# Performance work log

Measured on AMD Instinct MI355X. Metric: run time of the kernel, lower is better.

## Reference

```python
import jax, jax.numpy as jnp
import numpy as np

B, T, D = 2, 2048, 1024
H, DK, DV = 16, 64, 64
FF = 4096


def setup_inputs() -> dict:
    key = jax.random.key(0)
    ks = jax.random.split(key, 10)
    s = 0.02
    return {
        "x": jax.random.normal(ks[0], (B, T, D), dtype=jnp.float32),
        "Wq": jax.random.normal(ks[1], (H, D, DK), dtype=jnp.float32) * s,
        "Wk": jax.random.normal(ks[2], (H, D, DK), dtype=jnp.float32) * s,
        "Wv": jax.random.normal(ks[3], (H, D, DV), dtype=jnp.float32) * s,
        "Wo": jax.random.normal(ks[4], (D, D), dtype=jnp.float32) * s,
        "W1": jax.random.normal(ks[5], (D, FF), dtype=jnp.float32) * s,
        "b1": jnp.zeros((FF,), dtype=jnp.float32),
        "W2": jax.random.normal(ks[6], (FF, D), dtype=jnp.float32) * s,
        "b2": jnp.zeros((D,), dtype=jnp.float32),
    }


def _meanstd_norm(y):
    # torch: mean(-1), std(-1) with Bessel correction (ddof=1)
    mean = jnp.mean(y, axis=-1, keepdims=True)
    var = jnp.sum((y - mean) ** 2, axis=-1, keepdims=True) / (y.shape[-1] - 1)
    return (y - mean) / jnp.sqrt(var)


def reference(x, Wq, Wk, Wv, Wo, W1, b1, W2, b2):
    dk = Wq.shape[-1]
    # per-head projections: (B,T,D) x (H,D,dk) -> (B,H,T,dk)
    q = jnp.einsum('btd,hdk->bhtk', x, Wq)
    k = jnp.einsum('btd,hdk->bhtk', x, Wk)
    v = jnp.einsum('btd,hdv->bhtv', x, Wv)
    scores = jnp.einsum('bhqk,bhsk->bhqs', q, k) / np.sqrt(dk)
    # NOTE: softmax over dim=-2 (query axis), as in the original module
    attn = jax.nn.softmax(scores, axis=-2)
    o = jnp.einsum('bhqs,bhsv->bhqv', attn, v)  # (B,H,T,DV)
    o = o.transpose(0, 2, 1, 3).reshape(o.shape[0], o.shape[2], -1)  # (B,T,H*DV)
    o = o @ Wo
    out1 = _meanstd_norm(o + x)
    ff = jax.nn.relu(out1 @ W1 + b1) @ W2 + b2
    out2 = _meanstd_norm(ff + out1)
    return out2
```

## Files before the change

kernel.cpp:

```cpp
#include <hip/hip_runtime.h>
#include <hip/hip_bf16.h>
#include <math.h>

#define B_  2
#define T_  2048
#define D_  1024
#define H_  16
#define DK_ 64
#define FF_ 4096
#define BT_ (B_*T_)

typedef __attribute__((ext_vector_type(8))) short bf16x8;
typedef __attribute__((ext_vector_type(4))) float f32x4;

__device__ __forceinline__ ushort f2bf(float f) {
    __hip_bfloat16 h = __float2bfloat16(f);
    return *reinterpret_cast<ushort*>(&h);
}
__device__ __forceinline__ float bf2f(ushort u) {
    __hip_bfloat16 h;
    *reinterpret_cast<ushort*>(&h) = u;
    return __bfloat162float(h);
}

__device__ __forceinline__ void g2l16(const ushort* g, ushort* l) {
    __builtin_amdgcn_global_load_lds(
        (const __attribute__((address_space(1))) void*)g,
        (__attribute__((address_space(3))) void*)l, 16, 0, 0);
}

__global__ __launch_bounds__(256) void cvt_bf16_kernel(
    const float* __restrict__ in, ushort* __restrict__ out, int n)
{
    int i = (blockIdx.x * 256 + threadIdx.x) * 4;
    if (i >= n) return;
    float4 v = *(const float4*)(in + i);
    ushort4 o;
    o.x = f2bf(v.x); o.y = f2bf(v.y); o.z = f2bf(v.z); o.w = f2bf(v.w);
    *(ushort4*)(out + i) = o;
}

__global__ __launch_bounds__(256) void transpose_bf16_kernel(
    const float* __restrict__ in, ushort* __restrict__ out,
    int K, int N, long in_bstride, long out_bstride)
{
    __shared__ float t[32][33];
    const float* ib = in + (size_t)blockIdx.z * in_bstride;
    ushort* ob = out + (size_t)blockIdx.z * out_bstride;
    int n0 = blockIdx.x * 32, k0 = blockIdx.y * 32;
    int tid = threadIdx.x;
    int r = tid >> 3, c4 = (tid & 7) * 4;
    float4 v = *(const float4*)(ib + (size_t)(k0 + r) * N + n0 + c4);
    t[r][c4] = v.x; t[r][c4+1] = v.y; t[r][c4+2] = v.z; t[r][c4+3] = v.w;
    __syncthreads();
    int n = tid >> 3, kc = (tid & 7) * 4;
    ushort4 o;
    o.x = f2bf(t[kc+0][n]); o.y = f2bf(t[kc+1][n]);
    o.z = f2bf(t[kc+2][n]); o.w = f2bf(t[kc+3][n]);
    *(ushort4*)(ob + (size_t)(n0 + n) * K + k0 + kc) = o;
}

template<int OUT_BF16>
__global__ __launch_bounds__(256, 2) void gemm_ntw_kernel(
    const ushort* __restrict__ A, int lda,
    const ushort* __restrict__ Bt, int ldb,
    void* __restrict__ C, int ldc, int K,
    const float* __restrict__ bias,
    const float* __restrict__ resid, int relu)
{
    __shared__ __attribute__((aligned(16))) ushort As[2][4][128][8];
    __shared__ __attribute__((aligned(16))) ushort Bs[2][4][256][8];

    int nwg  = gridDim.x * gridDim.y;
    int orig = blockIdx.y * gridDim.x + blockIdx.x;
    int work = (orig & 7) * (nwg >> 3) + (orig >> 3);
    int bx = work % gridDim.x, by = work / gridDim.x;

    int row0 = by * 128, col0 = bx * 256;
    int tid = threadIdx.x;
    int w = tid >> 6, l = tid & 63;
    int wr = (w >> 1) * 64, wc = (w & 1) * 128;

    int m0 = tid & 127, kc0 = tid >> 7;
    const ushort* gA = A  + (size_t)(row0 + m0) * lda + kc0 * 8;
    const ushort* gB = Bt + (size_t)(col0 + tid) * ldb;

    f32x4 acc[4][8];
    #pragma unroll
    for (int i = 0; i < 4; ++i)
        #pragma unroll
        for (int j = 0; j < 8; ++j) acc[i][j] = (f32x4){0.f, 0.f, 0.f, 0.f};

    const int NT = K >> 5;
    g2l16(gA,      &As[0][kc0    ][m0][0]);
    g2l16(gA + 16, &As[0][kc0 + 2][m0][0]);
    #pragma unroll
    for (int p = 0; p < 4; ++p)
        g2l16(gB + p*8, &Bs[0][p][tid][0]);
    __syncthreads();

    int cur = 0;
    for (int t = 0; t < NT; ++t) {
        if (t + 1 < NT) {
            int k0 = (t + 1) << 5;
            g2l16(gA + k0,      &As[cur ^ 1][kc0    ][m0][0]);
            g2l16(gA + k0 + 16, &As[cur ^ 1][kc0 + 2][m0][0]);
            #pragma unroll
            for (int p = 0; p < 4; ++p)
                g2l16(gB + k0 + p*8, &Bs[cur ^ 1][p][tid][0]);
        }
        int kc = l >> 4;
        bf16x8 bfr[8];
        #pragma unroll
        for (int j = 0; j < 8; ++j)
            bfr[j] = *(const bf16x8*)&Bs[cur][kc][wc + j*16 + (l & 15)][0];
        #pragma unroll
        for (int i = 0; i < 4; ++i) {
            bf16x8 a = *(const bf16x8*)&As[cur][kc][wr + i*16 + (l & 15)][0];
            #pragma unroll
            for (int j = 0; j < 8; ++j)
                acc[i][j] = __builtin_amdgcn_mfma_f32_16x16x32_bf16(
                    a, bfr[j], acc[i][j], 0, 0, 0);
        }
        __syncthreads();
        cur ^= 1;
    }

    #pragma unroll
    for (int i = 0; i < 4; ++i) {
        int rbase = row0 + wr + i*16 + (l >> 4) * 4;
        #pragma unroll
        for (int j = 0; j < 8; ++j) {
            int col = col0 + wc + j*16 + (l & 15);
            float bv = bias ? bias[col] : 0.f;
            #pragma unroll
            for (int r = 0; r < 4; ++r) {
                int row = rbase + r;
                float val = acc[i][j][r] + bv;
                if (resid) val += resid[(size_t)row * ldc + col];
                if (relu)  val = fmaxf(val, 0.f);
                if (OUT_BF16) ((ushort*)C)[(size_t)row * ldc + col] = f2bf(val);
                else          ((float*)C)[(size_t)row * ldc + col]  = val;
            }
        }
    }
}

template<int OUT_BF16>
__global__ __launch_bounds__(256) void gemm_nt_kernel(
    const ushort* __restrict__ A, int lda,
    const ushort* __restrict__ Bt, int ldb,
    void* __restrict__ C, int ldc, int K,
    const float* __restrict__ bias,
    const float* __restrict__ resid, int relu,
    long aZoff, long bZoff, long cZoff)
{
    __shared__ __attribute__((aligned(16))) ushort As[2][4][128][8];
    __shared__ __attribute__((aligned(16))) ushort Bs[2][4][128][8];

    A  += (size_t)blockIdx.z * aZoff;
    Bt += (size_t)blockIdx.z * bZoff;
    char* Cb = (char*)C + (size_t)blockIdx.z * cZoff * (OUT_BF16 ? 2 : 4);

    int nwg  = gridDim.x * gridDim.y;
    int orig = blockIdx.y * gridDim.x + blockIdx.x;
    int work = (orig & 7) * (nwg >> 3) + (orig >> 3);
    int bx = work % gridDim.x, by = work / gridDim.x;

    int row0 = by * 128, col0 = bx * 128;
    int tid = threadIdx.x;
    int w = tid >> 6, l = tid & 63;
    int wr = (w >> 1) * 64, wc = (w & 1) * 64;

    int m0 = tid & 127, kc0 = tid >> 7;
    const ushort* ga0 = A  + (size_t)(row0 + m0) * lda + kc0 * 8;
    const ushort* gb0 = Bt + (size_t)(col0 + m0) * ldb + kc0 * 8;

    f32x4 acc[4][4];
    #pragma unroll
    for (int i = 0; i < 4; ++i)
        #pragma unroll
        for (int j = 0; j < 4; ++j) acc[i][j] = (f32x4){0.f, 0.f, 0.f, 0.f};

    const int NT = K >> 5;
    g2l16(ga0,      &As[0][kc0    ][m0][0]);
    g2l16(ga0 + 16, &As[0][kc0 + 2][m0][0]);
    g2l16(gb0,      &Bs[0][kc0    ][m0][0]);
    g2l16(gb0 + 16, &Bs[0][kc0 + 2][m0][0]);
    __syncthreads();

    int cur = 0;
    for (int t = 0; t < NT; ++t) {
        if (t + 1 < NT) {
            int k0 = (t + 1) << 5;
            g2l16(ga0 + k0,      &As[cur ^ 1][kc0    ][m0][0]);
            g2l16(ga0 + k0 + 16, &As[cur ^ 1][kc0 + 2][m0][0]);
            g2l16(gb0 + k0,      &Bs[cur ^ 1][kc0    ][m0][0]);
            g2l16(gb0 + k0 + 16, &Bs[cur ^ 1][kc0 + 2][m0][0]);
        }
        int kc = l >> 4;
        bf16x8 af[4], bfr[4];
        #pragma unroll
        for (int i = 0; i < 4; ++i)
            af[i] = *(const bf16x8*)&As[cur][kc][wr + i*16 + (l & 15)][0];
        #pragma unroll
        for (int j = 0; j < 4; ++j)
            bfr[j] = *(const bf16x8*)&Bs[cur][kc][wc + j*16 + (l & 15)][0];
        #pragma unroll
        for (int i = 0; i < 4; ++i)
            #pragma unroll
            for (int j = 0; j < 4; ++j)
                acc[i][j] = __builtin_amdgcn_mfma_f32_16x16x32_bf16(
                    af[i], bfr[j], acc[i][j], 0, 0, 0);
        __syncthreads();
        cur ^= 1;
    }

    #pragma unroll
    for (int i = 0; i < 4; ++i) {
        int rbase = row0 + wr + i*16 + (l >> 4) * 4;
        #pragma unroll
        for (int j = 0; j < 4; ++j) {
            int col = col0 + wc + j*16 + (l & 15);
            float bv = bias ? bias[col] : 0.f;
            #pragma unroll
            for (int r = 0; r < 4; ++r) {
                int row = rbase + r;
                float val = acc[i][j][r] + bv;
                if (resid) val += resid[(size_t)row * ldc + col];
                if (relu)  val = fmaxf(val, 0.f);
                if (OUT_BF16) ((ushort*)Cb)[(size_t)row * ldc + col] = f2bf(val);
                else          ((float*)Cb)[(size_t)row * ldc + col]  = val;
            }
        }
    }
}

__global__ __launch_bounds__(256) void csumv_kernel(
    const ushort* __restrict__ qkv, ushort* __restrict__ vt)
{
    int bh = blockIdx.y, b = bh >> 4, h = bh & 15;
    int s0 = blockIdx.x * 128;
    const ushort* qb = qkv + (size_t)b * T_ * 3072 + h * 64;
    const ushort* kb = qb + 1024;
    const ushort* vb = qb + 2048;
    __shared__ __attribute__((aligned(16))) ushort Ks[8][128][8];
    __shared__ __attribute__((aligned(16))) ushort Qs[8][64][8];
    __shared__ float csl[128];
    __shared__ float t[64][65];
    int tid = threadIdx.x, w = tid >> 6, l = tid & 63;
    int scol = w * 32;

    #pragma unroll
    for (int p = 0; p < 4; ++p) {
        int idx = tid + p * 256;
        int s = idx & 127, kc = idx >> 7;
        *(uint4*)&Ks[kc][s][0] =
            *(const uint4*)(kb + (size_t)(s0 + s) * 3072 + kc * 8);
    }
    float cs[2] = {0.f, 0.f};
    for (int qt = 0; qt < T_ / 64; ++qt) {
        __syncthreads();
        #pragma unroll
        for (int p = 0; p < 2; ++p) {
            int idx = tid + p * 256;
            int qq = idx & 63, kc = idx >> 6;
            *(uint4*)&Qs[kc][qq][0] =
                *(const uint4*)(qb + (size_t)(qt*64 + qq) * 3072 + kc * 8);
        }
        __syncthreads();
        bf16x8 af[4][2], bfr[2][2];
        #pragma unroll
        for (int qi = 0; qi < 4; ++qi)
            #pragma unroll
            for (int ks = 0; ks < 2; ++ks)
                af[qi][ks] = *(const bf16x8*)&Qs[ks*4 + (l>>4)][qi*16 + (l & 15)][0];
        #pragma unroll
        for (int sj = 0; sj < 2; ++sj)
            #pragma unroll
            for (int ks = 0; ks < 2; ++ks)
                bfr[sj][ks] = *(const bf16x8*)&Ks[ks*4 + (l>>4)][scol + sj*16 + (l & 15)][0];
        #pragma unroll
        for (int qi = 0; qi < 4; ++qi)
            #pragma unroll
            for (int sj = 0; sj < 2; ++sj) {
                f32x4 d = (f32x4){0.f, 0.f, 0.f, 0.f};
                #pragma unroll
                for (int ks = 0; ks < 2; ++ks)
                    d = __builtin_amdgcn_mfma_f32_16x16x32_bf16(
                        af[qi][ks], bfr[sj][ks], d, 0, 0, 0);
                cs[sj] += __expf(d[0]*0.125f) + __expf(d[1]*0.125f)
                        + __expf(d[2]*0.125f) + __expf(d[3]*0.125f);
            }
    }
    #pragma unroll
    for (int sj = 0; sj < 2; ++sj) {
        float v = cs[sj];
        v += __shfl_down(v, 32, 64);
        v += __shfl_down(v, 16, 64);
        if (l < 16) csl[scol + sj*16 + l] = v;
    }
    __syncthreads();

    #pragma unroll
    for (int p2 = 0; p2 < 2; ++p2) {
        int sb = s0 + p2 * 64;
        #pragma unroll
        for (int p = 0; p < 2; ++p) {
            int idx = tid + p * 256;
            int s = idx >> 3, c0 = (idx & 7) * 8;
            uint4 raw = *(const uint4*)(vb + (size_t)(sb + s) * 3072 + c0);
            float rc = 1.0f / csl[p2 * 64 + s];
            ushort* u = (ushort*)&raw;
            #pragma unroll
            for (int i = 0; i < 8; ++i) t[s][c0 + i] = bf2f(u[i]) * rc;
        }
        __syncthreads();
        #pragma unroll
        for (int p = 0; p < 2; ++p) {
            int idx = tid + p * 256;
            int dv = idx >> 3, sc = (idx & 7) * 8;
            ushort o[8];
            #pragma unroll
            for (int i = 0; i < 8; ++i) o[i] = f2bf(t[sc + i][dv]);
            *(uint4*)(vt + ((size_t)bh * 64 + dv) * T_ + sb + sc) = *(uint4*)o;
        }
        __syncthreads();
    }
}

__global__ __launch_bounds__(256) void attn_pv_kernel(
    const ushort* __restrict__ qkv, const ushort* __restrict__ vt,
    ushort* __restrict__ attn_o)
{
    int bh = blockIdx.y, b = bh >> 4, h = bh & 15;
    int q0 = blockIdx.x * 64;
    const ushort* qb = qkv + (size_t)b * T_ * 3072 + h * 64;
    const ushort* kb = qb + 1024;
    const ushort* vtb = vt + (size_t)bh * 64 * T_;
    __shared__ __attribute__((aligned(16))) ushort Qs[8][64][8];
    __shared__ __attribute__((aligned(16))) ushort Ks[8][64][8];
    __shared__ __attribute__((aligned(16))) ushort Vs[8][64][8];
    __shared__ __attribute__((aligned(16))) ushort Es[8][64][8];
    int tid = threadIdx.x, w = tid >> 6, l = tid & 63;
    int qw = w * 16;

    #pragma unroll
    for (int p = 0; p < 2; ++p) {
        int idx = tid + p * 256;
        int qq = idx & 63, kc = idx >> 6;
        *(uint4*)&Qs[kc][qq][0] =
            *(const uint4*)(qb + (size_t)(q0 + qq) * 3072 + kc * 8);
    }
    __syncthreads();
    bf16x8 qf[2];
    #pragma unroll
    for (int ks = 0; ks < 2; ++ks)
        qf[ks] = *(const bf16x8*)&Qs[ks*4 + (l>>4)][qw + (l & 15)][0];

    f32x4 oacc[4];
    #pragma unroll
    for (int j = 0; j < 4; ++j) oacc[j] = (f32x4){0.f, 0.f, 0.f, 0.f};

    for (int st = 0; st < T_ / 64; ++st) {
        int s0 = st * 64;
        __syncthreads();
        #pragma unroll
        for (int p = 0; p < 2; ++p) {
            int idx = tid + p * 256;
            int rr = idx & 63, kc = idx >> 6;
            *(uint4*)&Ks[kc][rr][0] =
                *(const uint4*)(kb + (size_t)(s0 + rr) * 3072 + kc * 8);
            *(uint4*)&Vs[kc][rr][0] =
                *(const uint4*)(vtb + (size_t)rr * T_ + s0 + kc * 8);
        }
        __syncthreads();
        #pragma unroll
        for (int sj = 0; sj < 4; ++sj) {
            f32x4 d = (f32x4){0.f, 0.f, 0.f, 0.f};
            #pragma unroll
            for (int ks = 0; ks < 2; ++ks) {
                bf16x8 kf = *(const bf16x8*)&Ks[ks*4 + (l>>4)][sj*16 + (l & 15)][0];
                d = __builtin_amdgcn_mfma_f32_16x16x32_bf16(qf[ks], kf, d, 0, 0, 0);
            }
            #pragma unroll
            for (int r = 0; r < 4; ++r) {
                int qq = qw + (l>>4)*4 + r;
                int ss = sj*16 + (l & 15);
                Es[ss >> 3][qq][ss & 7] = f2bf(__expf(d[r] * 0.125f));
            }
        }
        bf16x8 ef[2];
        #pragma unroll
        for (int ks = 0; ks < 2; ++ks)
            ef[ks] = *(const bf16x8*)&Es[ks*4 + (l>>4)][qw + (l & 15)][0];
        #pragma unroll
        for (int j = 0; j < 4; ++j)
            #pragma unroll
            for (int ks = 0; ks < 2; ++ks) {
                bf16x8 vf = *(const bf16x8*)&Vs[ks*4 + (l>>4)][j*16 + (l & 15)][0];
                oacc[j] = __builtin_amdgcn_mfma_f32_16x16x32_bf16(ef[ks], vf, oacc[j], 0, 0, 0);
            }
    }
    #pragma unroll
    for (int j = 0; j < 4; ++j)
        #pragma unroll
        for (int r = 0; r < 4; ++r) {
            int qq = q0 + qw + (l>>4)*4 + r;
            int dv = j*16 + (l & 15);
            attn_o[(size_t)(b*T_ + qq) * 1024 + h*64 + dv] = f2bf(oacc[j][r]);
        }
}

__device__ __forceinline__ float block_reduce_sum_256(float v, float* tmp)
{
    #pragma unroll
    for (int off = 32; off; off >>= 1) v += __shfl_down(v, off, 64);
    int lane = threadIdx.x & 63, w = threadIdx.x >> 6;
    __syncthreads();
    if (lane == 0) tmp[w] = v;
    __syncthreads();
    return tmp[0] + tmp[1] + tmp[2] + tmp[3];
}

template<int Z>
__global__ __launch_bounds__(256) void normZ_fused_kernel(
    const ushort* __restrict__ parts, long zoff,
    const float* __restrict__ bias, const float* __restrict__ resid,
    float* __restrict__ outf, ushort* __restrict__ outb)
{
    __shared__ float tmp[4];
    int row = blockIdx.x;
    int tid = threadIdx.x;
    int c0 = tid * 4;
    size_t idx = (size_t)row * D_ + c0;
    float vals[4] = {0.f, 0.f, 0.f, 0.f};
    #pragma unroll
    for (int z = 0; z < Z; ++z) {
        ushort4 p = *(const ushort4*)&parts[idx + (size_t)z * zoff];
        vals[0] += bf2f(p.x); vals[1] += bf2f(p.y);
        vals[2] += bf2f(p.z); vals[3] += bf2f(p.w);
    }
    float4 rv = *(const float4*)&resid[idx];
    vals[0] += rv.x; vals[1] += rv.y; vals[2] += rv.z; vals[3] += rv.w;
    if (bias) {
        float4 bv = *(const float4*)&bias[c0];
        vals[0] += bv.x; vals[1] += bv.y; vals[2] += bv.z; vals[3] += bv.w;
    }
    float s = vals[0] + vals[1] + vals[2] + vals[3];
    s = block_reduce_sum_256(s, tmp);
    float m = s * (1.0f / (float)D_);
    float sq = 0.f;
    #pragma unroll
    for (int i = 0; i < 4; ++i) { float c = vals[i] - m; sq += c * c; }
    sq = block_reduce_sum_256(sq, tmp);
    float rs = rsqrtf(sq * (1.0f / (float)(D_ - 1)));
    float4 o;
    o.x = (vals[0] - m) * rs; o.y = (vals[1] - m) * rs;
    o.z = (vals[2] - m) * rs; o.w = (vals[3] - m) * rs;
    *(float4*)&outf[idx] = o;
    if (outb) {
        ushort4 ob;
        ob.x = f2bf(o.x); ob.y = f2bf(o.y); ob.z = f2bf(o.z); ob.w = f2bf(o.w);
        *(ushort4*)&outb[idx] = ob;
    }
}

extern "C" void kernel_launch(void* const* d_in, const int* in_sizes, int n_in,
                              void* d_out, int out_size, void* d_ws, size_t ws_size,
                              hipStream_t stream)
{
    const float* x  = (const float*)d_in[0];
    const float* Wq = (const float*)d_in[1];
    const float* Wk = (const float*)d_in[2];
    const float* Wv = (const float*)d_in[3];
    const float* Wo = (const float*)d_in[4];
    const float* W1 = (const float*)d_in[5];
    const float* b1 = (const float*)d_in[6];
    const float* W2 = (const float*)d_in[7];
    const float* b2 = (const float*)d_in[8];
    float* out = (float*)d_out;

    const size_t MB = (size_t)1 << 20;
    char* base = (char*)d_ws;
    ushort* qkv    = (ushort*)(base +   0*MB);
    ushort* hid    = (ushort*)(base +   0*MB);
    ushort* xb     = (ushort*)(base +  24*MB);
    ushort* W2t    = (ushort*)(base +  32*MB);
    ushort* Wqkvt  = (ushort*)(base +  40*MB);
    ushort* wpart  = (ushort*)(base +  40*MB);
    ushort* vt     = (ushort*)(base +  46*MB);
    ushort* Wot    = (ushort*)(base +  55*MB);
    ushort* W1t    = (ushort*)(base +  57*MB);
    ushort* attn_o = (ushort*)(base +  65*MB);
    ushort* wopart = (ushort*)(base +  73*MB);
    ushort* out1b  = (ushort*)(base +  89*MB);
    float*  out1f  = (float*) (base +  97*MB);

    cvt_bf16_kernel<<<dim3(BT_*D_/1024), 256, 0, stream>>>(x, xb, BT_*D_);
    transpose_bf16_kernel<<<dim3(2, 32, 16), 256, 0, stream>>>(
        Wq, Wqkvt + 0*1048576, 1024, 64, 65536, 65536);
    transpose_bf16_kernel<<<dim3(2, 32, 16), 256, 0, stream>>>(
        Wk, Wqkvt + 1*1048576, 1024, 64, 65536, 65536);
    transpose_bf16_kernel<<<dim3(2, 32, 16), 256, 0, stream>>>(
        Wv, Wqkvt + 2*1048576, 1024, 64, 65536, 65536);
    transpose_bf16_kernel<<<dim3(32, 32, 1), 256, 0, stream>>>(
        Wo, Wot, 1024, 1024, 0, 0);
    transpose_bf16_kernel<<<dim3(128, 32, 1), 256, 0, stream>>>(
        W1, W1t, 1024, 4096, 0, 0);
    transpose_bf16_kernel<<<dim3(32, 128, 1), 256, 0, stream>>>(
        W2, W2t, 4096, 1024, 0, 0);

    gemm_ntw_kernel<1><<<dim3(3072/256, 4096/128), 256, 0, stream>>>(
        xb, 1024, Wqkvt, 1024, qkv, 3072, 1024, nullptr, nullptr, 0);
    csumv_kernel<<<dim3(T_/128, B_*H_), 256, 0, stream>>>(qkv, vt);
    attn_pv_kernel<<<dim3(T_/64, B_*H_), 256, 0, stream>>>(qkv, vt, attn_o);
    gemm_nt_kernel<1><<<dim3(1024/128, 4096/128, 2), 256, 0, stream>>>(
        attn_o, 1024, Wot, 1024, wopart, 1024, 512, nullptr, nullptr, 0,
        512, 512, (long)4096*1024);
    normZ_fused_kernel<2><<<dim3(BT_), 256, 0, stream>>>(
        wopart, (long)4096*1024, nullptr, x, out1f, out1b);
    gemm_ntw_kernel<1><<<dim3(4096/256, 4096/128), 256, 0, stream>>>(
        out1b, 1024, W1t, 1024, hid, 4096, 1024, b1, nullptr, 1);
    gemm_nt_kernel<1><<<dim3(1024/128, 4096/128, 2), 256, 0, stream>>>(
        hid, 4096, W2t, 4096, wpart, 1024, 2048, nullptr, nullptr, 0,
        2048, 2048, (long)4096*1024);
    normZ_fused_kernel<2><<<dim3(BT_), 256, 0, stream>>>(
        wpart, (long)4096*1024, b2, out1f, out, nullptr);
}
```

Before: 390.7 us.

## Double-buffer attention K/V/Q tiles with async loads and widen query tile

Both attention kernels now prefetch the next K/V (or Q) tile into a second LDS buffer with g2l16 asynchronous global-to-LDS copies while the current tile is computed. This replaces the two barriers per iteration with one and overlaps memory latency with MFMA and exp work. attn_pv also handles 128 queries per block, two 16-row query tiles per wave, with Q fragments read straight from global into registers. This doubles reuse of each staged K/V tile and halves the grid, at the cost of more LDS and registers per block and fewer blocks to spread across CUs.

```diff
diff --git a/kernel.cpp b/kernel.cpp
--- a/kernel.cpp
+++ b/kernel.cpp
@@ -245,11 +245,12 @@
     const ushort* kb = qb + 1024;
     const ushort* vb = qb + 2048;
     __shared__ __attribute__((aligned(16))) ushort Ks[8][128][8];
-    __shared__ __attribute__((aligned(16))) ushort Qs[8][64][8];
+    __shared__ __attribute__((aligned(16))) ushort Qs[2][8][64][8];
     __shared__ float csl[128];
     __shared__ float t[64][65];
     int tid = threadIdx.x, w = tid >> 6, l = tid & 63;
     int scol = w * 32;
+    int qq0 = l, kcA = w, kcB = w + 4;
 
     #pragma unroll
     for (int p = 0; p < 4; ++p) {
@@ -258,23 +259,24 @@
         *(uint4*)&Ks[kc][s][0] =
             *(const uint4*)(kb + (size_t)(s0 + s) * 3072 + kc * 8);
     }
+    g2l16(qb + (size_t)qq0 * 3072 + kcA * 8, &Qs[0][kcA][qq0][0]);
+    g2l16(qb + (size_t)qq0 * 3072 + kcB * 8, &Qs[0][kcB][qq0][0]);
+    __syncthreads();
+
     float cs[2] = {0.f, 0.f};
+    int cur = 0;
     for (int qt = 0; qt < T_ / 64; ++qt) {
-        __syncthreads();
-        #pragma unroll
-        for (int p = 0; p < 2; ++p) {
-            int idx = tid + p * 256;
-            int qq = idx & 63, kc = idx >> 6;
-            *(uint4*)&Qs[kc][qq][0] =
-                *(const uint4*)(qb + (size_t)(qt*64 + qq) * 3072 + kc * 8);
-        }
-        __syncthreads();
+        if (qt + 1 < T_ / 64) {
+            const ushort* qn = qb + (size_t)((qt + 1) * 64 + qq0) * 3072;
+            g2l16(qn + kcA * 8, &Qs[cur ^ 1][kcA][qq0][0]);
+            g2l16(qn + kcB * 8, &Qs[cur ^ 1][kcB][qq0][0]);
+        }
         bf16x8 af[4][2], bfr[2][2];
         #pragma unroll
         for (int qi = 0; qi < 4; ++qi)
             #pragma unroll
             for (int ks = 0; ks < 2; ++ks)
-                af[qi][ks] = *(const bf16x8*)&Qs[ks*4 + (l>>4)][qi*16 + (l & 15)][0];
+                af[qi][ks] = *(const bf16x8*)&Qs[cur][ks*4 + (l>>4)][qi*16 + (l & 15)][0];
         #pragma unroll
         for (int sj = 0; sj < 2; ++sj)
             #pragma unroll
@@ -292,6 +294,8 @@
                 cs[sj] += __expf(d[0]*0.125f) + __expf(d[1]*0.125f)
                         + __expf(d[2]*0.125f) + __expf(d[3]*0.125f);
             }
+        __syncthreads();
+        cur ^= 1;
     }
     #pragma unroll
     for (int sj = 0; sj < 2; ++sj) {
@@ -334,82 +338,95 @@
     ushort* __restrict__ attn_o)
 {
     int bh = blockIdx.y, b = bh >> 4, h = bh & 15;
-    int q0 = blockIdx.x * 64;
+    int q0 = blockIdx.x * 128;
     const ushort* qb = qkv + (size_t)b * T_ * 3072 + h * 64;
     const ushort* kb = qb + 1024;
     const ushort* vtb = vt + (size_t)bh * 64 * T_;
-    __shared__ __attribute__((aligned(16))) ushort Qs[8][64][8];
-    __shared__ __attribute__((aligned(16))) ushort Ks[8][64][8];
-    __shared__ __attribute__((aligned(16))) ushort Vs[8][64][8];
-    __shared__ __attribute__((aligned(16))) ushort Es[8][64][8];
+    __shared__ __attribute__((aligned(16))) ushort Ks[2][8][64][8];
+    __shared__ __attribute__((aligned(16))) ushort Vs[2][8][64][8];
+    __shared__ __attribute__((aligned(16))) ushort Es[8][128][8];
     int tid = threadIdx.x, w = tid >> 6, l = tid & 63;
-    int qw = w * 16;
-
-    #pragma unroll
-    for (int p = 0; p < 2; ++p) {
-        int idx = tid + p * 256;
-        int qq = idx & 63, kc = idx >> 6;
-        *(uint4*)&Qs[kc][qq][0] =
-            *(const uint4*)(qb + (size_t)(q0 + qq) * 3072 + kc * 8);
-    }
-    __syncthreads();
-    bf16x8 qf[2];
-    #pragma unroll
-    for (int ks = 0; ks < 2; ++ks)
-        qf[ks] = *(const bf16x8*)&Qs[ks*4 + (l>>4)][qw + (l & 15)][0];
-
-    f32x4 oacc[4];
-    #pragma unroll
-    for (int j = 0; j < 4; ++j) oacc[j] = (f32x4){0.f, 0.f, 0.f, 0.f};
-
-    for (int st = 0; st < T_ / 64; ++st) {
-        int s0 = st * 64;
+    int wq = w * 32;
+
+    int kcA = w, kcB = w + 4;
+
+    bf16x8 qf[2][2];
+    #pragma unroll
+    for (int qt = 0; qt < 2; ++qt)
+        #pragma unroll
+        for (int ks = 0; ks < 2; ++ks)
+            qf[qt][ks] = *(const bf16x8*)(qb
+                + (size_t)(q0 + wq + qt*16 + (l & 15)) * 3072
+                + (ks*4 + (l >> 4)) * 8);
+
+    f32x4 oacc[2][4];
+    #pragma unroll
+    for (int qt = 0; qt < 2; ++qt)
+        #pragma unroll
+        for (int j = 0; j < 4; ++j) oacc[qt][j] = (f32x4){0.f, 0.f, 0.f, 0.f};
+
+    const int NT = T_ / 64;
+    g2l16(kb + (size_t)l * 3072 + kcA * 8, &Ks[0][kcA][l][0]);
+    g2l16(kb + (size_t)l * 3072 + kcB * 8, &Ks[0][kcB][l][0]);
+    g2l16(vtb + (size_t)l * T_ + kcA * 8,  &Vs[0][kcA][l][0]);
+    g2l16(vtb + (size_t)l * T_ + kcB * 8,  &Vs[0][kcB][l][0]);
+    __syncthreads();
+
+    int cur = 0;
+    for (int st = 0; st < NT; ++st) {
+        if (st + 1 < NT) {
+            int s1 = (st + 1) * 64;
+            g2l16(kb + (size_t)(s1 + l) * 3072 + kcA * 8, &Ks[cur^1][kcA][l][0]);
+            g2l16(kb + (size_t)(s1 + l) * 3072 + kcB * 8, &Ks[cur^1][kcB][l][0]);
+            g2l16(vtb + (size_t)l * T_ + s1 + kcA * 8,    &Vs[cur^1][kcA][l][0]);
+            g2l16(vtb + (size_t)l * T_ + s1 + kcB * 8,    &Vs[cur^1][kcB][l][0]);
+        }
+        #pragma unroll
+        for (int qt = 0; qt < 2; ++qt)
+            #pragma unroll
+            for (int sj = 0; sj < 4; ++sj) {
+                f32x4 d = (f32x4){0.f, 0.f, 0.f, 0.f};
+                #pragma unroll
+                for (int ks = 0; ks < 2; ++ks) {
+                    bf16x8 kf = *(const bf16x8*)&Ks[cur][ks*4 + (l>>4)][sj*16 + (l & 15)][0];
+                    d = __builtin_amdgcn_mfma_f32_16x16x32_bf16(qf[qt][ks], kf, d, 0, 0, 0);
+                }
+                #pragma unroll
+                for (int r = 0; r < 4; ++r) {
+                    int qq = wq + qt*16 + (l>>4)*4 + r;
+                    int ss = sj*16 + (l & 15);
+                    Es[ss >> 3][qq][ss & 7] = f2bf(__expf(d[r] * 0.125f));
+                }
+            }
+        #pragma unroll
+        for (int qt = 0; qt < 2; ++qt) {
+            bf16x8 ef[2];
+            #pragma unroll
+            for (int ks = 0; ks < 2; ++ks)
+                ef[ks] = *(const bf16x8*)&Es[ks*4 + (l>>4)][wq + qt*16 + (l & 15)][0];
+            #pragma unroll
+            for (int j = 0; j < 4; ++j)
+                #pragma unroll
+                for (int ks = 0; ks < 2; ++ks) {
+                    bf16x8 vf = *(const bf16x8*)&Vs[cur][ks*4 + (l>>4)][j*16 + (l & 15)][0];
+                    oacc[qt][j] = __builtin_amdgcn_mfma_f32_16x16x32_bf16(
+                        ef[ks], vf, oacc[qt][j], 0, 0, 0);
+                }
+        }
         __syncthreads();
-        #pragma unroll
-        for (int p = 0; p < 2; ++p) {
-            int idx = tid + p * 256;
-            int rr = idx & 63, kc = idx >> 6;
-            *(uint4*)&Ks[kc][rr][0] =
-                *(const uint4*)(kb + (size_t)(s0 + rr) * 3072 + kc * 8);
-            *(uint4*)&Vs[kc][rr][0] =
-                *(const uint4*)(vtb + (size_t)rr * T_ + s0 + kc * 8);
-        }
-        __syncthreads();
-        #pragma unroll
-        for (int sj = 0; sj < 4; ++sj) {
-            f32x4 d = (f32x4){0.f, 0.f, 0.f, 0.f};
-            #pragma unroll
-            for (int ks = 0; ks < 2; ++ks) {
-                bf16x8 kf = *(const bf16x8*)&Ks[ks*4 + (l>>4)][sj*16 + (l & 15)][0];
-                d = __builtin_amdgcn_mfma_f32_16x16x32_bf16(qf[ks], kf, d, 0, 0, 0);
+        cur ^= 1;
+    }
+
+    #pragma unroll
+    for (int qt = 0; qt < 2; ++qt)
+        #pragma unroll
+        for (int j = 0; j < 4; ++j)
+            #pragma unroll
+            for (int r = 0; r < 4; ++r) {
+                int qq = q0 + wq + qt*16 + (l>>4)*4 + r;
+                int dv = j*16 + (l & 15);
+                attn_o[(size_t)(b*T_ + qq) * 1024 + h*64 + dv] = f2bf(oacc[qt][j][r]);
             }
-            #pragma unroll
-            for (int r = 0; r < 4; ++r) {
-                int qq = qw + (l>>4)*4 + r;
-                int ss = sj*16 + (l & 15);
-                Es[ss >> 3][qq][ss & 7] = f2bf(__expf(d[r] * 0.125f));
-            }
-        }
-        bf16x8 ef[2];
-        #pragma unroll
-        for (int ks = 0; ks < 2; ++ks)
-            ef[ks] = *(const bf16x8*)&Es[ks*4 + (l>>4)][qw + (l & 15)][0];
-        #pragma unroll
-        for (int j = 0; j < 4; ++j)
-            #pragma unroll
-            for (int ks = 0; ks < 2; ++ks) {
-                bf16x8 vf = *(const bf16x8*)&Vs[ks*4 + (l>>4)][j*16 + (l & 15)][0];
-                oacc[j] = __builtin_amdgcn_mfma_f32_16x16x32_bf16(ef[ks], vf, oacc[j], 0, 0, 0);
-            }
-    }
-    #pragma unroll
-    for (int j = 0; j < 4; ++j)
-        #pragma unroll
-        for (int r = 0; r < 4; ++r) {
-            int qq = q0 + qw + (l>>4)*4 + r;
-            int dv = j*16 + (l & 15);
-            attn_o[(size_t)(b*T_ + qq) * 1024 + h*64 + dv] = f2bf(oacc[j][r]);
-        }
 }
 
 __device__ __forceinline__ float block_reduce_sum_256(float v, float* tmp)
@@ -514,7 +531,7 @@
     gemm_ntw_kernel<1><<<dim3(3072/256, 4096/128), 256, 0, stream>>>(
         xb, 1024, Wqkvt, 1024, qkv, 3072, 1024, nullptr, nullptr, 0);
     csumv_kernel<<<dim3(T_/128, B_*H_), 256, 0, stream>>>(qkv, vt);
-    attn_pv_kernel<<<dim3(T_/64, B_*H_), 256, 0, stream>>>(qkv, vt, attn_o);
+    attn_pv_kernel<<<dim3(T_/128, B_*H_), 256, 0, stream>>>(qkv, vt, attn_o);
     gemm_nt_kernel<1><<<dim3(1024/128, 4096/128, 2), 256, 0, stream>>>(
         attn_o, 1024, Wot, 1024, wopart, 1024, 512, nullptr, nullptr, 0,
         512, 512, (long)4096*1024);
```

Result: no change. 390.6 us (-0.0%).
